# Kernel optimization log

Hardware: AMD Instinct MI355X
Metric: run time of the kernel (lower is better)

The kernel has to match this reference:

```python
import jax, jax.numpy as jnp
import numpy as np
from functools import reduce

N_QUBITS = 12          # input_shape[-2] = 2**12 = 4096; must be multiple of 4
DIM = 2 ** N_QUBITS
N_GATES = N_QUBITS // 4  # one diamond U-gate (4 qubits, 16x16) per group
BATCH = 128
TWO_PI = 6.283185307179586


def setup_inputs() -> dict:
    key = jax.random.key(0)
    k1, k2, k3, k4 = jax.random.split(key, 4)
    thetas = jax.random.uniform(k1, (N_GATES,), jnp.float32, 0.0, TWO_PI)
    # Fixed Hermitian generator for the 16x16 gate, pre-diagonalized:
    # U(theta) = V @ diag(exp(-i*theta*evals)) @ V^T
    rng = np.random.RandomState(42)
    H = rng.randn(16, 16).astype(np.float32)
    H = (H + H.T) * 0.5
    evals_np, evecs_np = np.linalg.eigh(H)
    evecs = jnp.asarray(evecs_np, jnp.float32)
    evals = jnp.asarray(evals_np, jnp.float32)
    state_real = jax.random.normal(k3, (BATCH, DIM, 1), jnp.float32)
    state_imag = jax.random.normal(k4, (BATCH, DIM, 1), jnp.float32)
    return {"thetas": thetas, "evecs": evecs, "evals": evals,
            "state_real": state_real, "state_imag": state_imag}


def _gate(theta, evecs, evals):
    # 16x16 unitary: V diag(exp(-i theta lambda)) V^T  (V real orthogonal)
    phase = jnp.exp(-1j * (theta * evals).astype(jnp.complex64))  # [16]
    V = evecs.astype(jnp.complex64)
    return (V * phase[None, :]) @ V.T  # [16,16] complex64


def reference(thetas, evecs, evals, state_real, state_imag):
    # Build each 4-qubit gate, then the full unitary via Kronecker product
    Us = [_gate(thetas[i], evecs, evals) for i in range(N_GATES)]
    U_full = reduce(jnp.kron, Us)  # [DIM, DIM] complex64 (the anti-pattern)
    psi = state_real.astype(jnp.complex64) + 1j * state_imag.astype(jnp.complex64)
    out = jnp.einsum('ij,bjk->bik', U_full, psi)  # U @ inputs
    # stack real/imag so output is a single real array: [2, BATCH, DIM, 1]
    return jnp.stack([jnp.real(out), jnp.imag(out)])
```

## Files before the change

### kernel.cpp

```cpp
#include <hip/hip_runtime.h>

#define DIM 4096
#define NB 128

__global__ __launch_bounds__(256)
void ulayer_a(const float* __restrict__ thetas,
              const float* __restrict__ evecs,
              const float* __restrict__ evals,
              const float* __restrict__ sre,
              const float* __restrict__ sim,
              float2* __restrict__ ws)
{
    __shared__ float  sV[256];
    __shared__ float  sC[32], sS[32];
    __shared__ float2 sG1[16][17];
    __shared__ float2 sG2[16][17];
    __shared__ float2 x0[16][17];
    __shared__ float2 x1[16][17];

    const int t  = threadIdx.x;
    const int b  = blockIdx.x >> 4;
    const int c  = blockIdx.x & 15;
    const int i1 = t >> 4;
    const int i2 = t & 15;

    sV[t] = evecs[t];
    if (t < 32) {
        const int g = (t >> 4) + 1;
        const int k = t & 15;
        float sn, cs;
        sincosf(thetas[g] * evals[k], &sn, &cs);
        sC[t] = cs;
        sS[t] = sn;
    }

    const int d = b * DIM + c * 256 + t;
    const float xr = sre[d];
    const float xi = sim[d];
    x0[i1][i2] = make_float2(xr, xi);

    __syncthreads();

#pragma unroll
    for (int rep = 0; rep < 2; ++rep) {
        const int e  = t + (rep << 8);
        const int gg = e >> 8;
        const int i  = (e >> 4) & 15;
        const int j  = e & 15;
        float gr = 0.f, gi = 0.f;
#pragma unroll
        for (int k = 0; k < 16; ++k) {
            const float vv = sV[i * 16 + k] * sV[j * 16 + k];
            gr = fmaf(vv,  sC[(gg << 4) + k], gr);
            gi = fmaf(vv, -sS[(gg << 4) + k], gi);
        }
        if (gg == 0) sG1[i][j] = make_float2(gr, gi);
        else         sG2[j][i] = make_float2(gr, gi);
    }
    __syncthreads();

    {
        float ar = 0.f, ai = 0.f;
#pragma unroll
        for (int j = 0; j < 16; ++j) {
            const float2 g = sG2[j][i2];
            const float2 x = x0[i1][j];
            ar = fmaf(g.x,  x.x, ar);
            ar = fmaf(-g.y, x.y, ar);
            ai = fmaf(g.x,  x.y, ai);
            ai = fmaf(g.y,  x.x, ai);
        }
        x1[i1][i2] = make_float2(ar, ai);
    }
    __syncthreads();

    {
        float ar = 0.f, ai = 0.f;
#pragma unroll
        for (int j = 0; j < 16; ++j) {
            const float2 g = sG1[i1][j];
            const float2 x = x1[j][i2];
            ar = fmaf(g.x,  x.x, ar);
            ar = fmaf(-g.y, x.y, ar);
            ai = fmaf(g.x,  x.y, ai);
            ai = fmaf(g.y,  x.x, ai);
        }
        ws[d] = make_float2(ar, ai);
    }
}

__global__ __launch_bounds__(256)
void ulayer_b(const float* __restrict__ thetas,
              const float* __restrict__ evecs,
              const float* __restrict__ evals,
              const float2* __restrict__ ws,
              float* __restrict__ out)
{
    __shared__ float  sV[256];
    __shared__ float  sC[16], sS[16];
    __shared__ float2 sG0[16][16];

    const int t  = threadIdx.x;
    const int b  = blockIdx.x >> 2;
    const int fp = blockIdx.x & 3;
    const int q  = t >> 6;
    const int fl = t & 63;
    const int f  = fp * 64 + fl;

    float2 x[16];
    const float2* __restrict__ wsb = ws + (size_t)b * DIM;
#pragma unroll
    for (int j = 0; j < 16; ++j) x[j] = wsb[j * 256 + f];

    sV[t] = evecs[t];
    if (t < 16) {
        float sn, cs;
        sincosf(thetas[0] * evals[t], &sn, &cs);
        sC[t] = cs;
        sS[t] = sn;
    }
    __syncthreads();

    {
        const int i = t >> 4, j = t & 15;
        float gr = 0.f, gi = 0.f;
#pragma unroll
        for (int k = 0; k < 16; ++k) {
            const float vv = sV[i * 16 + k] * sV[j * 16 + k];
            gr = fmaf(vv,  sC[k], gr);
            gi = fmaf(vv, -sS[k], gi);
        }
        sG0[i][j] = make_float2(gr, gi);
    }
    __syncthreads();

    float* __restrict__ ore = out + (size_t)b * DIM;
    float* __restrict__ oim = out + (size_t)NB * DIM + (size_t)b * DIM;

#pragma unroll
    for (int r = 0; r < 4; ++r) {
        const int i0 = q * 4 + r;
        float ar = 0.f, ai = 0.f;
#pragma unroll
        for (int j = 0; j < 16; ++j) {
            const float2 g = sG0[i0][j];
            ar = fmaf(g.x,  x[j].x, ar);
            ar = fmaf(-g.y, x[j].y, ar);
            ai = fmaf(g.x,  x[j].y, ai);
            ai = fmaf(g.y,  x[j].x, ai);
        }
        const int od = i0 * 256 + f;
        ore[od] = ar;
        oim[od] = ai;
    }
}

extern "C" void kernel_launch(void* const* d_in, const int* in_sizes, int n_in,
                              void* d_out, int out_size, void* d_ws, size_t ws_size,
                              hipStream_t stream) {
    const float* thetas = (const float*)d_in[0];
    const float* evecs  = (const float*)d_in[1];
    const float* evals  = (const float*)d_in[2];
    const float* sre    = (const float*)d_in[3];
    const float* sim    = (const float*)d_in[4];
    float* outp = (float*)d_out;
    float2* ws  = (float2*)d_ws;

    ulayer_a<<<NB * 16, 256, 0, stream>>>(thetas, evecs, evals, sre, sim, ws);
    ulayer_b<<<NB * 4,  256, 0, stream>>>(thetas, evecs, evals, ws, outp);
}
```

Before: 79.57 us.

## Fuse both gate-layer kernels into one and drop the workspace round trip

Replaces the two-kernel pipeline, which wrote an intermediate complex state to a global workspace, with one kernel. Each block builds all three 16x16 gates in shared memory and applies them to a quarter of one batch row's middle-gate output rows, passing intermediates through padded shared tiles. This removes one launch and the global write and reread of the intermediate. In exchange, each block rereads the whole input row (four times redundant, mostly from L2), the gates are rebuilt per block, and the grid shrinks to 512 blocks.

```diff
diff --git a/kernel.cpp b/kernel.cpp
--- a/kernel.cpp
+++ b/kernel.cpp
@@ -2,156 +2,128 @@
 
 #define DIM 4096
 #define NB 128
+#define P 17
 
 __global__ __launch_bounds__(256)
-void ulayer_a(const float* __restrict__ thetas,
-              const float* __restrict__ evecs,
-              const float* __restrict__ evals,
-              const float* __restrict__ sre,
-              const float* __restrict__ sim,
-              float2* __restrict__ ws)
+void ulayer_fused(const float* __restrict__ thetas,
+                  const float* __restrict__ evecs,
+                  const float* __restrict__ evals,
+                  const float* __restrict__ sre,
+                  const float* __restrict__ sim,
+                  float* __restrict__ out)
 {
     __shared__ float  sV[256];
-    __shared__ float  sC[32], sS[32];
-    __shared__ float2 sG1[16][17];
-    __shared__ float2 sG2[16][17];
-    __shared__ float2 x0[16][17];
-    __shared__ float2 x1[16][17];
+    __shared__ float  sC[48], sS[48];
+    __shared__ float2 sG[3][16][16];
+    __shared__ float2 A[16][4][P];
+    __shared__ float2 B[4][16][P];
 
     const int t  = threadIdx.x;
-    const int b  = blockIdx.x >> 4;
-    const int c  = blockIdx.x & 15;
-    const int i1 = t >> 4;
+    const int b  = blockIdx.x >> 2;
+    const int qq = blockIdx.x & 3;
+
+    const int i0 = t >> 4;
     const int i2 = t & 15;
+    const float* __restrict__ pr = sre + (size_t)b * DIM + i0 * 256 + i2;
+    const float* __restrict__ pi = sim + (size_t)b * DIM + i0 * 256 + i2;
+    float xr[16], xi[16];
+#pragma unroll
+    for (int j = 0; j < 16; ++j) { xr[j] = pr[j * 16]; xi[j] = pi[j * 16]; }
 
     sV[t] = evecs[t];
-    if (t < 32) {
-        const int g = (t >> 4) + 1;
-        const int k = t & 15;
+    if (t < 48) {
+        const int g = t >> 4, k = t & 15;
         float sn, cs;
         sincosf(thetas[g] * evals[k], &sn, &cs);
         sC[t] = cs;
         sS[t] = sn;
     }
-
-    const int d = b * DIM + c * 256 + t;
-    const float xr = sre[d];
-    const float xi = sim[d];
-    x0[i1][i2] = make_float2(xr, xi);
-
     __syncthreads();
 
 #pragma unroll
-    for (int rep = 0; rep < 2; ++rep) {
-        const int e  = t + (rep << 8);
-        const int gg = e >> 8;
-        const int i  = (e >> 4) & 15;
-        const int j  = e & 15;
+    for (int rep = 0; rep < 3; ++rep) {
+        const int e = t + (rep << 8);
+        const int g = e >> 8;
+        const int i = (e >> 4) & 15;
+        const int j = e & 15;
         float gr = 0.f, gi = 0.f;
 #pragma unroll
         for (int k = 0; k < 16; ++k) {
             const float vv = sV[i * 16 + k] * sV[j * 16 + k];
-            gr = fmaf(vv,  sC[(gg << 4) + k], gr);
-            gi = fmaf(vv, -sS[(gg << 4) + k], gi);
+            gr = fmaf(vv,  sC[(g << 4) + k], gr);
+            gi = fmaf(vv, -sS[(g << 4) + k], gi);
         }
-        if (gg == 0) sG1[i][j] = make_float2(gr, gi);
-        else         sG2[j][i] = make_float2(gr, gi);
+        sG[g][i][j] = make_float2(gr, gi);
+    }
+    __syncthreads();
+
+#pragma unroll
+    for (int l = 0; l < 4; ++l) {
+        float ar = 0.f, ai = 0.f;
+#pragma unroll
+        for (int j = 0; j < 16; ++j) {
+            const float2 g = sG[1][qq * 4 + l][j];
+            ar = fmaf(g.x,  xr[j], ar);
+            ar = fmaf(-g.y, xi[j], ar);
+            ai = fmaf(g.x,  xi[j], ai);
+            ai = fmaf(g.y,  xr[j], ai);
+        }
+        A[i0][l][i2] = make_float2(ar, ai);
     }
     __syncthreads();
 
     {
-        float ar = 0.f, ai = 0.f;
+        const int ig  = t >> 6;
+        const int fid = t & 63;
+        const int fi0 = fid >> 2;
+        const int fl  = fid & 3;
+        float2 x2[16];
 #pragma unroll
-        for (int j = 0; j < 16; ++j) {
-            const float2 g = sG2[j][i2];
-            const float2 x = x0[i1][j];
-            ar = fmaf(g.x,  x.x, ar);
-            ar = fmaf(-g.y, x.y, ar);
-            ai = fmaf(g.x,  x.y, ai);
-            ai = fmaf(g.y,  x.x, ai);
+        for (int j = 0; j < 16; ++j) x2[j] = A[fi0][fl][j];
+#pragma unroll
+        for (int q = 0; q < 4; ++q) {
+            const int r = ig * 4 + q;
+            float ar = 0.f, ai = 0.f;
+#pragma unroll
+            for (int j = 0; j < 16; ++j) {
+                const float2 g = sG[2][r][j];
+                ar = fmaf(g.x,  x2[j].x, ar);
+                ar = fmaf(-g.y, x2[j].y, ar);
+                ai = fmaf(g.x,  x2[j].y, ai);
+                ai = fmaf(g.y,  x2[j].x, ai);
+            }
+            B[fl][r][fi0] = make_float2(ar, ai);
         }
-        x1[i1][i2] = make_float2(ar, ai);
     }
     __syncthreads();
 
     {
-        float ar = 0.f, ai = 0.f;
+        const int rg = t >> 6;
+        const int fl = t & 63;
+        const int l   = fl >> 4;
+        const int i2f = fl & 15;
+        float2 x0[16];
 #pragma unroll
-        for (int j = 0; j < 16; ++j) {
-            const float2 g = sG1[i1][j];
-            const float2 x = x1[j][i2];
-            ar = fmaf(g.x,  x.x, ar);
-            ar = fmaf(-g.y, x.y, ar);
-            ai = fmaf(g.x,  x.y, ai);
-            ai = fmaf(g.y,  x.x, ai);
+        for (int j = 0; j < 16; ++j) x0[j] = B[l][i2f][j];
+
+        float* __restrict__ ore = out + (size_t)b * DIM;
+        float* __restrict__ oim = out + (size_t)NB * DIM + (size_t)b * DIM;
+#pragma unroll
+        for (int r = 0; r < 4; ++r) {
+            const int ro = rg * 4 + r;
+            float ar = 0.f, ai = 0.f;
+#pragma unroll
+            for (int j = 0; j < 16; ++j) {
+                const float2 g = sG[0][ro][j];
+                ar = fmaf(g.x,  x0[j].x, ar);
+                ar = fmaf(-g.y, x0[j].y, ar);
+                ai = fmaf(g.x,  x0[j].y, ai);
+                ai = fmaf(g.y,  x0[j].x, ai);
+            }
+            const int od = ro * 256 + (qq * 4 + l) * 16 + i2f;
+            ore[od] = ar;
+            oim[od] = ai;
         }
-        ws[d] = make_float2(ar, ai);
-    }
-}
-
-__global__ __launch_bounds__(256)
-void ulayer_b(const float* __restrict__ thetas,
-              const float* __restrict__ evecs,
-              const float* __restrict__ evals,
-              const float2* __restrict__ ws,
-              float* __restrict__ out)
-{
-    __shared__ float  sV[256];
-    __shared__ float  sC[16], sS[16];
-    __shared__ float2 sG0[16][16];
-
-    const int t  = threadIdx.x;
-    const int b  = blockIdx.x >> 2;
-    const int fp = blockIdx.x & 3;
-    const int q  = t >> 6;
-    const int fl = t & 63;
-    const int f  = fp * 64 + fl;
-
-    float2 x[16];
-    const float2* __restrict__ wsb = ws + (size_t)b * DIM;
-#pragma unroll
-    for (int j = 0; j < 16; ++j) x[j] = wsb[j * 256 + f];
-
-    sV[t] = evecs[t];
-    if (t < 16) {
-        float sn, cs;
-        sincosf(thetas[0] * evals[t], &sn, &cs);
-        sC[t] = cs;
-        sS[t] = sn;
-    }
-    __syncthreads();
-
-    {
-        const int i = t >> 4, j = t & 15;
-        float gr = 0.f, gi = 0.f;
-#pragma unroll
-        for (int k = 0; k < 16; ++k) {
-            const float vv = sV[i * 16 + k] * sV[j * 16 + k];
-            gr = fmaf(vv,  sC[k], gr);
-            gi = fmaf(vv, -sS[k], gi);
-        }
-        sG0[i][j] = make_float2(gr, gi);
-    }
-    __syncthreads();
-
-    float* __restrict__ ore = out + (size_t)b * DIM;
-    float* __restrict__ oim = out + (size_t)NB * DIM + (size_t)b * DIM;
-
-#pragma unroll
-    for (int r = 0; r < 4; ++r) {
-        const int i0 = q * 4 + r;
-        float ar = 0.f, ai = 0.f;
-#pragma unroll
-        for (int j = 0; j < 16; ++j) {
-            const float2 g = sG0[i0][j];
-            ar = fmaf(g.x,  x[j].x, ar);
-            ar = fmaf(-g.y, x[j].y, ar);
-            ai = fmaf(g.x,  x[j].y, ai);
-            ai = fmaf(g.y,  x[j].x, ai);
-        }
-        const int od = i0 * 256 + f;
-        ore[od] = ar;
-        oim[od] = ai;
     }
 }
 
@@ -164,8 +136,5 @@
     const float* sre    = (const float*)d_in[3];
     const float* sim    = (const float*)d_in[4];
     float* outp = (float*)d_out;
-    float2* ws  = (float2*)d_ws;
-
-    ulayer_a<<<NB * 16, 256, 0, stream>>>(thetas, evecs, evals, sre, sim, ws);
-    ulayer_b<<<NB * 4,  256, 0, stream>>>(thetas, evecs, evals, ws, outp);
+    ulayer_fused<<<NB * 4, 256, 0, stream>>>(thetas, evecs, evals, sre, sim, outp);
 }
```

After: 73.13 us. -8.1%, faster.
